# Performance work log

Hardware: AMD Instinct MI355X
Metric: run time of the kernel (lower is better)

Reference implementation:

```python
import jax, jax.numpy as jnp
import numpy as np

H, C = 5, 64            # attention heads, per-head channels (out_channels=conv_dim)
NEG_SLOPE = 0.2         # GATv2 leaky_relu slope
N_NODES = 50000

def setup_inputs() -> dict:
    key = jax.random.key(0)
    ks = jax.random.split(key, 10)
    N, E = N_NODES, 400000
    node_dim, edge_dim = 128, 16
    s = 0.1
    return {
        'x': jax.random.normal(ks[0], (N, node_dim), jnp.float32),
        'edge_index': jax.random.randint(ks[1], (2, E), 0, N),
        'edge_attr': jax.random.normal(ks[2], (E, edge_dim), jnp.float32),
        'W0': jax.random.normal(ks[3], (node_dim, H * C), jnp.float32) * s,
        'b0': jnp.zeros((H * C,), jnp.float32),
        'We0': jax.random.normal(ks[4], (edge_dim, H * C), jnp.float32) * s,
        'att0': jax.random.normal(ks[5], (H, C), jnp.float32) * s,
        'bias0': jnp.zeros((C,), jnp.float32),
        'W12': jax.random.normal(ks[6], (2, C, H * C), jnp.float32) * s,
        'b12': jnp.zeros((2, H * C), jnp.float32),
        'We12': jax.random.normal(ks[7], (2, edge_dim, H * C), jnp.float32) * s,
        'att12': jax.random.normal(ks[8], (2, H, C), jnp.float32) * s,
        'bias12': jnp.zeros((2, C), jnp.float32),
    }

def _add_self_loops_mean(edge_index, edge_attr, N):
    # PyG add_self_loops(fill_value='mean'): self-loop attr = mean of incoming edge attrs per dst node
    dst = edge_index[1]
    sums = jax.ops.segment_sum(edge_attr, dst, num_segments=N)
    cnt = jax.ops.segment_sum(jnp.ones((edge_attr.shape[0], 1), edge_attr.dtype), dst, num_segments=N)
    loop_attr = sums / jnp.maximum(cnt, 1.0)
    loop = jnp.arange(N, dtype=edge_index.dtype)
    ei = jnp.concatenate([edge_index, jnp.stack([loop, loop])], axis=1)
    ea = jnp.concatenate([edge_attr, loop_attr], axis=0)
    return ei, ea

def _gatv2_layer(x, src, dst, eattr, W, b, We, att, bias, N):
    h = (x @ W + b).reshape(N, H, C)                     # shared lin_l==lin_r (share_weights=True)
    e = (eattr @ We).reshape(-1, H, C)                   # lin_edge (no bias)
    s = jax.nn.leaky_relu(h[src] + h[dst] + e, NEG_SLOPE)  # [E', H, C]
    logits = jnp.einsum('ehc,hc->eh', s, att)            # [E', H]
    m = jax.ops.segment_max(logits, dst, num_segments=N)
    m = jnp.where(jnp.isfinite(m), m, 0.0)
    ex = jnp.exp(logits - m[dst])
    denom = jax.ops.segment_sum(ex, dst, num_segments=N) + 1e-16
    alpha = ex / denom[dst]                              # per-dst softmax (dropout off: eval mode)
    msg = h[src] * alpha[:, :, None]
    out = jax.ops.segment_sum(msg, dst, num_segments=N)  # [N, H, C]
    return out.mean(axis=1) + bias                       # concat=False -> head mean, then bias

def reference(x, edge_index, edge_attr, W0, b0, We0, att0, bias0, W12, b12, We12, att12, bias12):
    N = x.shape[0]
    ei, ea = _add_self_loops_mean(edge_index, edge_attr, N)
    src, dst = ei[0], ei[1]
    h = jax.nn.elu(_gatv2_layer(x, src, dst, ea, W0, b0, We0, att0, bias0, N))
    for i in range(2):
        h = jax.nn.elu(_gatv2_layer(h, src, dst, ea, W12[i], b12[i], We12[i], att12[i], bias12[i], N))
    return h  # jk_mode='last'
```

## Files before the change

kernel.cpp:

```cpp
#include <hip/hip_runtime.h>
#include <hip/hip_fp16.h>
#include <math.h>

#define NH 5
#define NC 64
#define ED 16
#define HC 320
#define CH 32

typedef _Float16 h2  __attribute__((ext_vector_type(2)));
typedef _Float16 v4h __attribute__((ext_vector_type(4)));
typedef _Float16 v8h __attribute__((ext_vector_type(8)));
typedef float    v4f __attribute__((ext_vector_type(4)));

__device__ __forceinline__ float wave_sum_all(float x) {
    asm("v_add_f32_dpp %0, %1, %0 quad_perm:[1,0,3,2] row_mask:0xf bank_mask:0xf"
        : "+v"(x) : "v"(x));
    asm("v_add_f32_dpp %0, %1, %0 quad_perm:[2,3,0,1] row_mask:0xf bank_mask:0xf"
        : "+v"(x) : "v"(x));
    asm("v_add_f32_dpp %0, %1, %0 row_half_mirror row_mask:0xf bank_mask:0xf"
        : "+v"(x) : "v"(x));
    asm("v_add_f32_dpp %0, %1, %0 row_mirror row_mask:0xf bank_mask:0xf"
        : "+v"(x) : "v"(x));
    asm("v_add_f32_dpp %0, %1, %0 row_bcast:15 row_mask:0xa bank_mask:0xf"
        : "+v"(x) : "v"(x));
    asm("v_add_f32_dpp %0, %1, %0 row_bcast:31 row_mask:0xc bank_mask:0xf"
        : "+v"(x) : "v"(x));
    return __int_as_float(__builtin_amdgcn_readlane(__float_as_int(x), 63));
}


__global__ void count_kernel(const int* __restrict__ dst, int* __restrict__ cnt, int E) {
    int t = blockIdx.x * blockDim.x + threadIdx.x;
    if (t >= E) return;
    atomicAdd(&cnt[dst[t]], 1);
}

__global__ void scan1_kernel(const int* __restrict__ cnt, int* __restrict__ offsets,
                             int* __restrict__ blockSums, int N) {
    __shared__ int sh[1024];
    int i = blockIdx.x * 1024 + threadIdx.x;
    int v = (i < N) ? cnt[i] + 1 : 0;
    sh[threadIdx.x] = v;
    __syncthreads();
    for (int o = 1; o < 1024; o <<= 1) {
        int t = (threadIdx.x >= o) ? sh[threadIdx.x - o] : 0;
        __syncthreads();
        sh[threadIdx.x] += t;
        __syncthreads();
    }
    if (i < N) offsets[i] = sh[threadIdx.x] - v;
    if (threadIdx.x == 1023) blockSums[blockIdx.x] = sh[1023];
}

__global__ void scan2_kernel(int* __restrict__ blockSums, int nb) {
    if (threadIdx.x != 0 || blockIdx.x != 0) return;
    int run = 0;
    for (int j = 0; j < nb; ++j) {
        int v = blockSums[j];
        blockSums[j] = run;
        run += v;
    }
    blockSums[nb] = run;
}

__global__ void scan3_kernel(int* __restrict__ offsets, int* __restrict__ cursor,
                             const int* __restrict__ blockSums, int* __restrict__ winStart,
                             int N, int nb) {
    int i = blockIdx.x * blockDim.x + threadIdx.x;
    if (i >= N) return;
    int off = offsets[i] + blockSums[i >> 10];
    offsets[i] = off;
    cursor[i] = off;
    atomicMin(&winStart[off / CH], i);
    if (i == 0) offsets[N] = blockSums[nb];
}

__global__ void scatter_kernel(const int* __restrict__ src, const int* __restrict__ dst,
                               const float* __restrict__ ea, int* __restrict__ cursor,
                               int* __restrict__ srcs, h2* __restrict__ easrt,
                               int* __restrict__ selfSlot, int N, int E) {
    int t = blockIdx.x * blockDim.x + threadIdx.x;
    if (t >= E + N) return;
    int d, s;
    if (t < E) { d = dst[t]; s = src[t]; }
    else       { d = t - E; s = t - E; }
    int pos = atomicAdd(&cursor[d], 1);
    srcs[pos] = s;
    if (t < E) {
        const float4* rp = (const float4*)(ea + (size_t)t * ED);
        float4 f0 = rp[0], f1 = rp[1], f2 = rp[2], f3 = rp[3];
        h2 o[8];
        o[0].x = (_Float16)f0.x; o[0].y = (_Float16)f0.y;
        o[1].x = (_Float16)f0.z; o[1].y = (_Float16)f0.w;
        o[2].x = (_Float16)f1.x; o[2].y = (_Float16)f1.y;
        o[3].x = (_Float16)f1.z; o[3].y = (_Float16)f1.w;
        o[4].x = (_Float16)f2.x; o[4].y = (_Float16)f2.y;
        o[5].x = (_Float16)f2.z; o[5].y = (_Float16)f2.w;
        o[6].x = (_Float16)f3.x; o[6].y = (_Float16)f3.y;
        o[7].x = (_Float16)f3.z; o[7].y = (_Float16)f3.w;
        float4* wp = (float4*)(easrt + (size_t)pos * 8);
        wp[0] = *(const float4*)&o[0];
        wp[1] = *(const float4*)&o[4];
    } else {
        selfSlot[d] = pos;
    }
}

__global__ void loop_fill(const int* __restrict__ offsets, const int* __restrict__ selfSlot,
                          h2* __restrict__ easrt, int N) {
    int t = blockIdx.x * blockDim.x + threadIdx.x;
    int n = t >> 3, k2 = t & 7;
    if (n >= N) return;
    int beg = offsets[n], end = offsets[n + 1];
    int ss = selfSlot[n];
    float sx = 0.f, sy = 0.f;
    for (int j = beg; j < end; ++j) {
        if (j == ss) continue;
        h2 v = easrt[(size_t)j * 8 + k2];
        sx += (float)v.x; sy += (float)v.y;
    }
    float inv = 1.f / (float)max(end - beg - 1, 1);
    h2 o; o.x = (_Float16)(sx * inv); o.y = (_Float16)(sy * inv);
    easrt[(size_t)ss * 8 + k2] = o;
}

__global__ void transpose_w3(const float* __restrict__ W0, const float* __restrict__ W12,
                             _Float16* __restrict__ Wt0, _Float16* __restrict__ Wt1,
                             _Float16* __restrict__ Wt2) {
    int t = blockIdx.x * blockDim.x + threadIdx.x;
    const int R0 = 320 * 128, R1 = 320 * 64;
    if (t < R0) {
        int k = t / 320, n = t % 320;
        Wt0[(size_t)n * 128 + k] = (_Float16)W0[t];
    } else if (t < R0 + R1) {
        int u = t - R0, k = u / 320, n = u % 320;
        Wt1[(size_t)n * 64 + k] = (_Float16)W12[u];
    } else if (t < R0 + 2 * R1) {
        int u = t - R0 - R1, k = u / 320, n = u % 320;
        Wt2[(size_t)n * 64 + k] = (_Float16)W12[64 * HC + u];
    }
}

__global__ __launch_bounds__(256) void gemm_mfma(const _Float16* __restrict__ Ah,
                                                 const float* __restrict__ Af,
                                                 const _Float16* __restrict__ Bt,
                                                 const float* __restrict__ bias,
                                                 _Float16* __restrict__ CoutA,
                                                 _Float16* __restrict__ CoutB, int M, int K) {
    int lane = threadIdx.x & 63;
    int wave = threadIdx.x >> 6;
    int m = lane & 15, quad = lane >> 4;
    int rowBase = (blockIdx.x * 4 + wave) * 16;
    if (rowBase >= M) return;

    v4f acc[20];
#pragma unroll
    for (int c = 0; c < 20; ++c) acc[c] = (v4f){0.f, 0.f, 0.f, 0.f};

    for (int k0 = 0; k0 < K; k0 += 32) {
        v8h a;
        if (Af) {
            const float* ap = &Af[(size_t)(rowBase + m) * K + k0 + quad * 8];
            float4 f0 = *(const float4*)ap;
            float4 f1 = *(const float4*)(ap + 4);
            a[0] = (_Float16)f0.x; a[1] = (_Float16)f0.y;
            a[2] = (_Float16)f0.z; a[3] = (_Float16)f0.w;
            a[4] = (_Float16)f1.x; a[5] = (_Float16)f1.y;
            a[6] = (_Float16)f1.z; a[7] = (_Float16)f1.w;
        } else {
            a = *(const v8h*)&Ah[(size_t)(rowBase + m) * K + k0 + quad * 8];
        }
#pragma unroll
        for (int c = 0; c < 20; ++c) {
            v8h b = *(const v8h*)&Bt[(size_t)(c * 16 + m) * K + k0 + quad * 8];
            acc[c] = __builtin_amdgcn_mfma_f32_16x16x32_f16(a, b, acc[c], 0, 0, 0);
        }
    }
    float bb[20];
#pragma unroll
    for (int c = 0; c < 20; ++c) bb[c] = bias[c * 16 + m];
#pragma unroll
    for (int r = 0; r < 4; ++r) {
        int row = rowBase + quad * 4 + r;
#pragma unroll
        for (int c03 = 0; c03 < 4; ++c03) {
            v4h o;
#pragma unroll
            for (int h = 0; h < 4; ++h) {
                int c = c03 + 4 * h;
                o[h] = (_Float16)(acc[c][r] + bb[c]);
            }
            int cw = c03 * 16 + m;
            *(v4h*)&CoutA[(((size_t)row) * 64 + cw) * 4] = o;
            int c4 = c03 + 16;
            CoutB[((size_t)row) * 64 + cw] = (_Float16)(acc[c4][r] + bb[c4]);
        }
    }
}

__global__ __launch_bounds__(256) void gat_fused(const _Float16* __restrict__ hA,
                                                 const _Float16* __restrict__ hB,
                                                 const int* __restrict__ offsets,
                                                 const int* __restrict__ srcs,
                                                 const h2* __restrict__ easrt,
                                                 const int* __restrict__ winStart,
                                                 const float* __restrict__ We,
                                                 const float* __restrict__ att,
                                                 const float* __restrict__ bias,
                                                 _Float16* __restrict__ outH,
                                                 float* __restrict__ outF,
                                                 int N, int R) {
    int lane = threadIdx.x & 63;
    int wave = (blockIdx.x * blockDim.x + threadIdx.x) >> 6;
    int totalWaves = (gridDim.x * blockDim.x) >> 6;
    const float L2E = 1.4426950408889634f;

    h2 we2[8 * NH];
#pragma unroll
    for (int k2 = 0; k2 < 8; ++k2)
#pragma unroll
        for (int h = 0; h < NH; ++h) {
            h2 w;
            w.x = (_Float16)We[(2 * k2) * HC + h * NC + lane];
            w.y = (_Float16)We[(2 * k2 + 1) * HC + h * NC + lane];
            we2[k2 * NH + h] = w;
        }
    float attc6[NH], attc4[NH];
#pragma unroll
    for (int h = 0; h < NH; ++h) {
        float a = att[h * NC + lane];
        attc6[h] = 0.6f * L2E * a;
        attc4[h] = 0.4f * L2E * a;
    }
    float bc = bias[lane];

    for (int w = wave; w * CH < R; w += totalWaves) {
        int i = winStart[w];
        if (i >= N) continue;
        int winEnd = w * CH + CH;
        for (; i < N; ++i) {
            int beg = offsets[i];
            if (beg >= winEnd) break;
            int end = offsets[i + 1];

            v4h hd4 = *(const v4h*)&hA[((size_t)i * 64 + lane) * 4];
            float hd[NH];
#pragma unroll
            for (int h = 0; h < 4; ++h) hd[h] = (float)hd4[h];
            hd[4] = (float)hB[(size_t)i * 64 + lane];

            float l[NH] = {}, acc[NH] = {};
            int t = beg;
            for (; t + 2 <= end; t += 2) {
                int s0 = srcs[t], s1 = srcs[t + 1];
                v4h hs0v = *(const v4h*)&hA[((size_t)s0 * 64 + lane) * 4];
                v4h hs1v = *(const v4h*)&hA[((size_t)s1 * 64 + lane) * 4];
                _Float16 hs0e = hB[(size_t)s0 * 64 + lane];
                _Float16 hs1e = hB[(size_t)s1 * 64 + lane];
                const h2* ap = easrt + (size_t)t * 8;
                h2 a0[8], a1[8];
#pragma unroll
                for (int k2 = 0; k2 < 8; ++k2) { a0[k2] = ap[k2]; a1[k2] = ap[8 + k2]; }
                __builtin_amdgcn_s_setprio(1);
                float hs0[NH], hs1[NH], p0[NH], p1[NH];
#pragma unroll
                for (int h = 0; h < 4; ++h) { hs0[h] = (float)hs0v[h]; hs1[h] = (float)hs1v[h]; }
                hs0[4] = (float)hs0e; hs1[4] = (float)hs1e;
#pragma unroll
                for (int h = 0; h < NH; ++h) {
                    float v0 = hs0[h] + hd[h];
                    float v1 = hs1[h] + hd[h];
#pragma unroll
                    for (int k2 = 0; k2 < 8; ++k2) {
                        v0 = __builtin_amdgcn_fdot2(a0[k2], we2[k2 * NH + h], v0, false);
                        v1 = __builtin_amdgcn_fdot2(a1[k2], we2[k2 * NH + h], v1, false);
                    }
                    p0[h] = fmaf(fabsf(v0), attc4[h], v0 * attc6[h]);
                    p1[h] = fmaf(fabsf(v1), attc4[h], v1 * attc6[h]);
                }
#pragma unroll
                for (int h = 0; h < NH; ++h) {
                    float pe0 = exp2f(wave_sum_all(p0[h]));
                    float pe1 = exp2f(wave_sum_all(p1[h]));
                    l[h] += pe0 + pe1;
                    acc[h] = fmaf(pe0, hs0[h], fmaf(pe1, hs1[h], acc[h]));
                }
                __builtin_amdgcn_s_setprio(0);
            }
            if (t < end) {
                int s0 = srcs[t];
                v4h hs0v = *(const v4h*)&hA[((size_t)s0 * 64 + lane) * 4];
                _Float16 hs0e = hB[(size_t)s0 * 64 + lane];
                const h2* ap = easrt + (size_t)t * 8;
                h2 a0[8];
#pragma unroll
                for (int k2 = 0; k2 < 8; ++k2) a0[k2] = ap[k2];
                float hs0[NH];
#pragma unroll
                for (int h = 0; h < 4; ++h) hs0[h] = (float)hs0v[h];
                hs0[4] = (float)hs0e;
#pragma unroll
                for (int h = 0; h < NH; ++h) {
                    float v0 = hs0[h] + hd[h];
#pragma unroll
                    for (int k2 = 0; k2 < 8; ++k2)
                        v0 = __builtin_amdgcn_fdot2(a0[k2], we2[k2 * NH + h], v0, false);
                    float pe0 = exp2f(wave_sum_all(fmaf(fabsf(v0), attc4[h], v0 * attc6[h])));
                    l[h] += pe0;
                    acc[h] = fmaf(pe0, hs0[h], acc[h]);
                }
            }
            float o = 0.f;
#pragma unroll
            for (int h = 0; h < NH; ++h) o += acc[h] / l[h];
            o = o * 0.2f + bc;
            o = o > 0.f ? o : expm1f(o);
            if (outF) outF[(size_t)i * NC + lane] = o;
            else      outH[(size_t)i * NC + lane] = (_Float16)o;
        }
    }
}

extern "C" void kernel_launch(void* const* d_in, const int* in_sizes, int n_in,
                              void* d_out, int out_size, void* d_ws, size_t ws_size,
                              hipStream_t stream) {
    const float* x     = (const float*)d_in[0];
    const int*   ei    = (const int*)d_in[1];
    const float* ea    = (const float*)d_in[2];
    const float* W0    = (const float*)d_in[3];
    const float* b0    = (const float*)d_in[4];
    const float* We0   = (const float*)d_in[5];
    const float* att0  = (const float*)d_in[6];
    const float* bias0 = (const float*)d_in[7];
    const float* W12   = (const float*)d_in[8];
    const float* b12   = (const float*)d_in[9];
    const float* We12  = (const float*)d_in[10];
    const float* att12 = (const float*)d_in[11];
    const float* bias12= (const float*)d_in[12];

    int N = in_sizes[0] / 128;
    int E = in_sizes[1] / 2;
    int R = E + N;
    int numWin = (R + CH - 1) / CH;
    int nb = (N + 1023) / 1024;
    const int* srcArr = ei;
    const int* dstArr = ei + E;

    char* ws = (char*)d_ws;
    size_t off = 0;
    auto alloc = [&](size_t bytes) -> void* {
        void* p = ws + off;
        off = (off + bytes + 255) & ~(size_t)255;
        return p;
    };
    int*      cnt     = (int*)alloc((size_t)N * 4);
    int*      offsets = (int*)alloc((size_t)(N + 1) * 4);
    int*      cursor  = (int*)alloc((size_t)N * 4);
    int*      selfSlot= (int*)alloc((size_t)N * 4);
    int*      blockSums=(int*)alloc((size_t)(nb + 1) * 4);
    _Float16* hbufA   = (_Float16*)alloc((size_t)N * 64 * 4 * 2);
    _Float16* hbufB   = (_Float16*)alloc((size_t)N * 64 * 2);
    _Float16* acth    = (_Float16*)alloc((size_t)N * NC * 2);
    _Float16* Wth0    = (_Float16*)alloc((size_t)320 * 128 * 2);
    _Float16* Wth1    = (_Float16*)alloc((size_t)320 * 64 * 2);
    _Float16* Wth2    = (_Float16*)alloc((size_t)320 * 64 * 2);
    int*      winStart= (int*)alloc((size_t)(numWin + 1) * 4);
    h2*       easrt   = (h2*)alloc((size_t)R * 32);
    int*      srcs    = (int*)alloc((size_t)R * 4);

    (void)hipMemsetAsync(cnt, 0, (size_t)N * 4, stream);
    (void)hipMemsetAsync(winStart, 0x7f, (size_t)(numWin + 1) * 4, stream);
    count_kernel<<<(E + 255) / 256, 256, 0, stream>>>(dstArr, cnt, E);
    scan1_kernel<<<nb, 1024, 0, stream>>>(cnt, offsets, blockSums, N);
    scan2_kernel<<<1, 64, 0, stream>>>(blockSums, nb);
    scan3_kernel<<<(N + 255) / 256, 256, 0, stream>>>(offsets, cursor, blockSums, winStart, N, nb);
    scatter_kernel<<<(E + N + 255) / 256, 256, 0, stream>>>(srcArr, dstArr, ea, cursor,
                                                            srcs, easrt, selfSlot, N, E);
    loop_fill<<<((size_t)N * 8 + 255) / 256, 256, 0, stream>>>(offsets, selfSlot, easrt, N);
    transpose_w3<<<(320 * 256 + 255) / 256, 256, 0, stream>>>(W0, W12, Wth0, Wth1, Wth2);

    float* dout = (float*)d_out;
    int gemmBlocks = (N / 16 + 3) / 4 + 1;
    int fusedBlocks = (numWin + 3) / 4;

    const _Float16* Ahs[3] = {nullptr, acth, acth};
    const float*    Afs[3] = {x, nullptr, nullptr};
    const _Float16* Bts[3] = {Wth0, Wth1, Wth2};
    int Ks[3] = {128, 64, 64};
    const float* bs[3]   = {b0, b12, b12 + HC};
    const float* Wes[3]  = {We0, We12, We12 + ED * HC};
    const float* atts[3] = {att0, att12, att12 + NH * NC};
    const float* bis[3]  = {bias0, bias12, bias12 + NC};
    for (int layer = 0; layer < 3; ++layer) {
        gemm_mfma<<<gemmBlocks, 256, 0, stream>>>(Ahs[layer], Afs[layer], Bts[layer], bs[layer],
                                                  hbufA, hbufB, N, Ks[layer]);
        gat_fused<<<fusedBlocks, 256, 0, stream>>>(hbufA, hbufB, offsets, srcs, easrt, winStart,
                                                   Wes[layer], atts[layer], bis[layer],
                                                   acth, (layer == 2) ? dout : nullptr, N, R);
    }
}
```

Baseline: 714.4 us.

## Split fused GAT edge kernel into edge-logit and node-aggregate passes

Result: slower. 886.4 us (+24.1%).

```diff
diff --git a/kernel.cpp b/kernel.cpp
--- a/kernel.cpp
+++ b/kernel.cpp
@@ -65,21 +65,20 @@
 }
 
 __global__ void scan3_kernel(int* __restrict__ offsets, int* __restrict__ cursor,
-                             const int* __restrict__ blockSums, int* __restrict__ winStart,
-                             int N, int nb) {
+                             const int* __restrict__ blockSums, int N, int nb) {
     int i = blockIdx.x * blockDim.x + threadIdx.x;
     if (i >= N) return;
     int off = offsets[i] + blockSums[i >> 10];
     offsets[i] = off;
     cursor[i] = off;
-    atomicMin(&winStart[off / CH], i);
     if (i == 0) offsets[N] = blockSums[nb];
 }
 
 __global__ void scatter_kernel(const int* __restrict__ src, const int* __restrict__ dst,
                                const float* __restrict__ ea, int* __restrict__ cursor,
-                               int* __restrict__ srcs, h2* __restrict__ easrt,
-                               int* __restrict__ selfSlot, int N, int E) {
+                               int* __restrict__ srcs, int* __restrict__ dsts,
+                               h2* __restrict__ easrt, int* __restrict__ selfSlot,
+                               int N, int E) {
     int t = blockIdx.x * blockDim.x + threadIdx.x;
     if (t >= E + N) return;
     int d, s;
@@ -87,6 +86,7 @@
     else       { d = t - E; s = t - E; }
     int pos = atomicAdd(&cursor[d], 1);
     srcs[pos] = s;
+    dsts[pos] = d;
     if (t < E) {
         const float4* rp = (const float4*)(ea + (size_t)t * ED);
         float4 f0 = rp[0], f1 = rp[1], f2 = rp[2], f3 = rp[3];
@@ -199,21 +199,16 @@
     }
 }
 
-__global__ __launch_bounds__(256) void gat_fused(const _Float16* __restrict__ hA,
-                                                 const _Float16* __restrict__ hB,
-                                                 const int* __restrict__ offsets,
-                                                 const int* __restrict__ srcs,
-                                                 const h2* __restrict__ easrt,
-                                                 const int* __restrict__ winStart,
-                                                 const float* __restrict__ We,
-                                                 const float* __restrict__ att,
-                                                 const float* __restrict__ bias,
-                                                 _Float16* __restrict__ outH,
-                                                 float* __restrict__ outF,
-                                                 int N, int R) {
+__global__ __launch_bounds__(256) void edge_logits(const _Float16* __restrict__ hA,
+                                                   const _Float16* __restrict__ hB,
+                                                   const int* __restrict__ srcs,
+                                                   const int* __restrict__ dsts,
+                                                   const h2* __restrict__ easrt,
+                                                   const float* __restrict__ We,
+                                                   const float* __restrict__ att,
+                                                   float* __restrict__ pe, int R) {
     int lane = threadIdx.x & 63;
     int wave = (blockIdx.x * blockDim.x + threadIdx.x) >> 6;
-    int totalWaves = (gridDim.x * blockDim.x) >> 6;
     const float L2E = 1.4426950408889634f;
 
     h2 we2[8 * NH];
@@ -233,93 +228,76 @@
         attc6[h] = 0.6f * L2E * a;
         attc4[h] = 0.4f * L2E * a;
     }
-    float bc = bias[lane];
-
-    for (int w = wave; w * CH < R; w += totalWaves) {
-        int i = winStart[w];
-        if (i >= N) continue;
-        int winEnd = w * CH + CH;
-        for (; i < N; ++i) {
-            int beg = offsets[i];
-            if (beg >= winEnd) break;
-            int end = offsets[i + 1];
-
-            v4h hd4 = *(const v4h*)&hA[((size_t)i * 64 + lane) * 4];
-            float hd[NH];
-#pragma unroll
-            for (int h = 0; h < 4; ++h) hd[h] = (float)hd4[h];
-            hd[4] = (float)hB[(size_t)i * 64 + lane];
-
-            float l[NH] = {}, acc[NH] = {};
-            int t = beg;
-            for (; t + 2 <= end; t += 2) {
-                int s0 = srcs[t], s1 = srcs[t + 1];
-                v4h hs0v = *(const v4h*)&hA[((size_t)s0 * 64 + lane) * 4];
-                v4h hs1v = *(const v4h*)&hA[((size_t)s1 * 64 + lane) * 4];
-                _Float16 hs0e = hB[(size_t)s0 * 64 + lane];
-                _Float16 hs1e = hB[(size_t)s1 * 64 + lane];
-                const h2* ap = easrt + (size_t)t * 8;
-                h2 a0[8], a1[8];
-#pragma unroll
-                for (int k2 = 0; k2 < 8; ++k2) { a0[k2] = ap[k2]; a1[k2] = ap[8 + k2]; }
-                __builtin_amdgcn_s_setprio(1);
-                float hs0[NH], hs1[NH], p0[NH], p1[NH];
-#pragma unroll
-                for (int h = 0; h < 4; ++h) { hs0[h] = (float)hs0v[h]; hs1[h] = (float)hs1v[h]; }
-                hs0[4] = (float)hs0e; hs1[4] = (float)hs1e;
-#pragma unroll
-                for (int h = 0; h < NH; ++h) {
-                    float v0 = hs0[h] + hd[h];
-                    float v1 = hs1[h] + hd[h];
-#pragma unroll
-                    for (int k2 = 0; k2 < 8; ++k2) {
-                        v0 = __builtin_amdgcn_fdot2(a0[k2], we2[k2 * NH + h], v0, false);
-                        v1 = __builtin_amdgcn_fdot2(a1[k2], we2[k2 * NH + h], v1, false);
-                    }
-                    p0[h] = fmaf(fabsf(v0), attc4[h], v0 * attc6[h]);
-                    p1[h] = fmaf(fabsf(v1), attc4[h], v1 * attc6[h]);
-                }
-#pragma unroll
-                for (int h = 0; h < NH; ++h) {
-                    float pe0 = exp2f(wave_sum_all(p0[h]));
-                    float pe1 = exp2f(wave_sum_all(p1[h]));
-                    l[h] += pe0 + pe1;
-                    acc[h] = fmaf(pe0, hs0[h], fmaf(pe1, hs1[h], acc[h]));
-                }
-                __builtin_amdgcn_s_setprio(0);
-            }
-            if (t < end) {
-                int s0 = srcs[t];
-                v4h hs0v = *(const v4h*)&hA[((size_t)s0 * 64 + lane) * 4];
-                _Float16 hs0e = hB[(size_t)s0 * 64 + lane];
-                const h2* ap = easrt + (size_t)t * 8;
-                h2 a0[8];
-#pragma unroll
-                for (int k2 = 0; k2 < 8; ++k2) a0[k2] = ap[k2];
-                float hs0[NH];
-#pragma unroll
-                for (int h = 0; h < 4; ++h) hs0[h] = (float)hs0v[h];
-                hs0[4] = (float)hs0e;
-#pragma unroll
-                for (int h = 0; h < NH; ++h) {
-                    float v0 = hs0[h] + hd[h];
-#pragma unroll
-                    for (int k2 = 0; k2 < 8; ++k2)
-                        v0 = __builtin_amdgcn_fdot2(a0[k2], we2[k2 * NH + h], v0, false);
-                    float pe0 = exp2f(wave_sum_all(fmaf(fabsf(v0), attc4[h], v0 * attc6[h])));
-                    l[h] += pe0;
-                    acc[h] = fmaf(pe0, hs0[h], acc[h]);
-                }
-            }
-            float o = 0.f;
-#pragma unroll
-            for (int h = 0; h < NH; ++h) o += acc[h] / l[h];
-            o = o * 0.2f + bc;
-            o = o > 0.f ? o : expm1f(o);
-            if (outF) outF[(size_t)i * NC + lane] = o;
-            else      outH[(size_t)i * NC + lane] = (_Float16)o;
-        }
-    }
+
+    int t0 = wave * CH;
+    if (t0 >= R) return;
+    int tEnd = min(t0 + CH, R);
+    for (int t = t0; t < tEnd; ++t) {
+        int s = srcs[t], d = dsts[t];
+        v4h hsv = *(const v4h*)&hA[((size_t)s * 64 + lane) * 4];
+        v4h hdv = *(const v4h*)&hA[((size_t)d * 64 + lane) * 4];
+        float hs4 = (float)hB[(size_t)s * 64 + lane];
+        float hd4 = (float)hB[(size_t)d * 64 + lane];
+        const h2* ap = easrt + (size_t)t * 8;
+        h2 a[8];
+#pragma unroll
+        for (int k2 = 0; k2 < 8; ++k2) a[k2] = ap[k2];
+        float pv[NH];
+#pragma unroll
+        for (int h = 0; h < NH; ++h) {
+            float v = (h < 4) ? ((float)hsv[h] + (float)hdv[h]) : (hs4 + hd4);
+#pragma unroll
+            for (int k2 = 0; k2 < 8; ++k2)
+                v = __builtin_amdgcn_fdot2(a[k2], we2[k2 * NH + h], v, false);
+            pv[h] = fmaf(fabsf(v), attc4[h], v * attc6[h]);
+        }
+        float e0 = exp2f(wave_sum_all(pv[0]));
+        float e1 = exp2f(wave_sum_all(pv[1]));
+        float e2 = exp2f(wave_sum_all(pv[2]));
+        float e3 = exp2f(wave_sum_all(pv[3]));
+        float e4 = exp2f(wave_sum_all(pv[4]));
+        if (lane == 0) {
+            float4 q; q.x = e0; q.y = e1; q.z = e2; q.w = e3;
+            *(float4*)&pe[(size_t)t * 8] = q;
+            pe[(size_t)t * 8 + 4] = e4;
+        }
+    }
+}
+
+__global__ __launch_bounds__(256) void node_aggregate(const _Float16* __restrict__ hA,
+                                                      const _Float16* __restrict__ hB,
+                                                      const int* __restrict__ offsets,
+                                                      const int* __restrict__ srcs,
+                                                      const float* __restrict__ pe,
+                                                      const float* __restrict__ bias,
+                                                      _Float16* __restrict__ outH,
+                                                      float* __restrict__ outF, int N) {
+    int lane = threadIdx.x & 63;
+    int node = (blockIdx.x * blockDim.x + threadIdx.x) >> 6;
+    if (node >= N) return;
+    int beg = offsets[node], end = offsets[node + 1];
+
+    float l[NH] = {}, acc[NH] = {};
+    for (int t = beg; t < end; ++t) {
+        int s = srcs[t];
+        v4h hsv = *(const v4h*)&hA[((size_t)s * 64 + lane) * 4];
+        float hs4 = (float)hB[(size_t)s * 64 + lane];
+        float4 q = *(const float4*)&pe[(size_t)t * 8];
+        float q4 = pe[(size_t)t * 8 + 4];
+        l[0] += q.x; l[1] += q.y; l[2] += q.z; l[3] += q.w; l[4] += q4;
+        acc[0] = fmaf(q.x, (float)hsv[0], acc[0]);
+        acc[1] = fmaf(q.y, (float)hsv[1], acc[1]);
+        acc[2] = fmaf(q.z, (float)hsv[2], acc[2]);
+        acc[3] = fmaf(q.w, (float)hsv[3], acc[3]);
+        acc[4] = fmaf(q4, hs4, acc[4]);
+    }
+    float o = 0.f;
+#pragma unroll
+    for (int h = 0; h < NH; ++h) o += acc[h] / l[h];
+    o = o * 0.2f + bias[lane];
+    o = o > 0.f ? o : expm1f(o);
+    if (outF) outF[(size_t)node * NC + lane] = o;
+    else      outH[(size_t)node * NC + lane] = (_Float16)o;
 }
 
 extern "C" void kernel_launch(void* const* d_in, const int* in_sizes, int n_in,
@@ -342,8 +320,8 @@
     int N = in_sizes[0] / 128;
     int E = in_sizes[1] / 2;
     int R = E + N;
-    int numWin = (R + CH - 1) / CH;
     int nb = (N + 1023) / 1024;
+    int numStrips = (R + CH - 1) / CH;
     const int* srcArr = ei;
     const int* dstArr = ei + E;
 
@@ -365,24 +343,25 @@
     _Float16* Wth0    = (_Float16*)alloc((size_t)320 * 128 * 2);
     _Float16* Wth1    = (_Float16*)alloc((size_t)320 * 64 * 2);
     _Float16* Wth2    = (_Float16*)alloc((size_t)320 * 64 * 2);
-    int*      winStart= (int*)alloc((size_t)(numWin + 1) * 4);
     h2*       easrt   = (h2*)alloc((size_t)R * 32);
     int*      srcs    = (int*)alloc((size_t)R * 4);
+    int*      dsts    = (int*)alloc((size_t)R * 4);
+    float*    pe      = (float*)alloc((size_t)R * 8 * 4);
 
     (void)hipMemsetAsync(cnt, 0, (size_t)N * 4, stream);
-    (void)hipMemsetAsync(winStart, 0x7f, (size_t)(numWin + 1) * 4, stream);
     count_kernel<<<(E + 255) / 256, 256, 0, stream>>>(dstArr, cnt, E);
     scan1_kernel<<<nb, 1024, 0, stream>>>(cnt, offsets, blockSums, N);
     scan2_kernel<<<1, 64, 0, stream>>>(blockSums, nb);
-    scan3_kernel<<<(N + 255) / 256, 256, 0, stream>>>(offsets, cursor, blockSums, winStart, N, nb);
+    scan3_kernel<<<(N + 255) / 256, 256, 0, stream>>>(offsets, cursor, blockSums, N, nb);
     scatter_kernel<<<(E + N + 255) / 256, 256, 0, stream>>>(srcArr, dstArr, ea, cursor,
-                                                            srcs, easrt, selfSlot, N, E);
+                                                            srcs, dsts, easrt, selfSlot, N, E);
     loop_fill<<<((size_t)N * 8 + 255) / 256, 256, 0, stream>>>(offsets, selfSlot, easrt, N);
     transpose_w3<<<(320 * 256 + 255) / 256, 256, 0, stream>>>(W0, W12, Wth0, Wth1, Wth2);
 
     float* dout = (float*)d_out;
     int gemmBlocks = (N / 16 + 3) / 4 + 1;
-    int fusedBlocks = (numWin + 3) / 4;
+    int logitBlocks = (numStrips + 3) / 4;
+    int aggBlocks = (N + 3) / 4;
 
     const _Float16* Ahs[3] = {nullptr, acth, acth};
     const float*    Afs[3] = {x, nullptr, nullptr};
@@ -395,8 +374,10 @@
     for (int layer = 0; layer < 3; ++layer) {
         gemm_mfma<<<gemmBlocks, 256, 0, stream>>>(Ahs[layer], Afs[layer], Bts[layer], bs[layer],
                                                   hbufA, hbufB, N, Ks[layer]);
-        gat_fused<<<fusedBlocks, 256, 0, stream>>>(hbufA, hbufB, offsets, srcs, easrt, winStart,
-                                                   Wes[layer], atts[layer], bis[layer],
-                                                   acth, (layer == 2) ? dout : nullptr, N, R);
-    }
-}
+        edge_logits<<<logitBlocks, 256, 0, stream>>>(hbufA, hbufB, srcs, dsts, easrt,
+                                                     Wes[layer], atts[layer], pe, R);
+        node_aggregate<<<aggBlocks, 256, 0, stream>>>(hbufA, hbufB, offsets, srcs, pe,
+                                                      bis[layer], acth,
+                                                      (layer == 2) ? dout : nullptr, N);
+    }
+}
```
